# Kernel tuning notes

Measured on AMD Instinct MI355X. Metric: run time of the kernel, lower is better.

The kernel has to match this reference:

```python
import jax, jax.numpy as jnp
import numpy as np

S, B, F, H, L = 256, 64, 512, 512, 4
INV_SQRT_H = float(1.0 / np.sqrt(H))


def _ln(x, g, b, eps=1e-5):
    # torch nn.LayerNorm: biased variance, eps=1e-5
    mu = jnp.mean(x, axis=-1, keepdims=True)
    var = jnp.var(x, axis=-1, keepdims=True)
    return (x - mu) * jax.lax.rsqrt(var + eps) * g + b


def setup_inputs() -> dict:
    key = jax.random.key(0)
    k1, k2 = jax.random.split(key)
    x = jax.random.normal(k1, (S, B, F), dtype=jnp.float32)  # time-major [S,B,F]
    W = jax.random.normal(k2, (L, 6, F, H), dtype=jnp.float32) * 0.02  # q,k,v,i,f,o
    b = jnp.zeros((L, 6, H), jnp.float32)
    ln_g = jnp.ones((L, 6, H), jnp.float32)
    ln_b = jnp.zeros((L, 6, H), jnp.float32)
    return {"x": x, "W": W, "b": b, "ln_g": ln_g, "ln_b": ln_b}


def reference(x, W, b, ln_g, ln_b):
    # Dropout is identity (eval mode / p effectively 0).
    def step(carry, x_t):
        h, c, n = carry  # each [L,B,H]
        layer_input = x_t  # [B,F]
        hs, cs, ns = [], [], []
        for l in range(L):
            # all 6 gate projections in one einsum: [6,B,H]
            z = jnp.einsum('bf,gfh->gbh', layer_input, W[l]) + b[l][:, None, :]
            z = z.at[1].multiply(INV_SQRT_H)  # k = Wk(x)/sqrt(H) before LN
            z = _ln(z, ln_g[l][:, None, :], ln_b[l][:, None, :])
            q, k, v = z[0], z[1], z[2]
            i = jax.nn.sigmoid(z[3])
            f = jax.nn.sigmoid(z[4])
            o = jax.nn.sigmoid(z[5])
            # (k[:,:,None] @ v[:,None,:]).sum(dim=1) == k.sum(-1,keepdims)*v
            kv_sum = jnp.sum(k, axis=-1, keepdims=True) * v
            c_l = f * c[l] + i * kv_sum
            n_l = f * n[l] + i * k
            n_hat = n_l / (jnp.linalg.norm(n_l, axis=-1, keepdims=True) + 1e-8)
            h_l = o * jnp.tanh(q * n_hat)
            if l > 0:  # residual_conn
                h_l = h_l + layer_input
            layer_input = h_l
            hs.append(h_l); cs.append(c_l); ns.append(n_l)
        h = jnp.stack(hs); c = jnp.stack(cs); n = jnp.stack(ns)
        return (h, c, n), h[-1]

    init = tuple(jnp.zeros((L, B, H), x.dtype) for _ in range(3))
    (h, c, n), out = jax.lax.scan(step, init, x)  # out: [S,B,H] time-major
    return out, h, c, n
```

## Files before the change

kernel.cpp:

```cpp
#include <hip/hip_runtime.h>


typedef unsigned short u16;
typedef unsigned int   u32;
typedef short s8v __attribute__((ext_vector_type(8)));
typedef float f4v __attribute__((ext_vector_type(4)));

#define S_    256
#define B_    64
#define F_    512
#define H_    512
#define L_    4
#define NG    3072
#define RALL  16384
#define CH    16
#define INV_SQRT_H 0.044194173824159216f

__device__ __forceinline__ float bu2f(u16 u) {
    union { u32 i; float f; } z; z.i = ((u32)u) << 16; return z.f;
}
__device__ __forceinline__ u16 f2bf(float f) {
    union { float f; u32 i; } z; z.f = f;
    u32 r = (z.i + 0x7FFFu + ((z.i >> 16) & 1u)) >> 16;
    return (u16)r;
}
__device__ __forceinline__ float sigm(float x)  { return 1.0f / (1.0f + __expf(-x)); }
__device__ __forceinline__ float tanhf_(float x){ return 2.0f / (1.0f + __expf(-2.0f * x)) - 1.0f; }
__device__ __forceinline__ float wred64(float v) {
    #pragma unroll
    for (int m = 1; m < 64; m <<= 1) v += __shfl_xor(v, m);
    return v;
}
__device__ __forceinline__ void gl_lds16(const u16* g, u16* l) {
    __builtin_amdgcn_global_load_lds((const __attribute__((address_space(1))) u32*)g,
                                     (__attribute__((address_space(3))) u32*)l, 16, 0, 0);
}
__device__ __forceinline__ void unp8(uint4 u, float* f) {
    f[0] = bu2f((u16)(u.x & 0xffff)); f[1] = bu2f((u16)(u.x >> 16));
    f[2] = bu2f((u16)(u.y & 0xffff)); f[3] = bu2f((u16)(u.y >> 16));
    f[4] = bu2f((u16)(u.z & 0xffff)); f[5] = bu2f((u16)(u.z >> 16));
    f[6] = bu2f((u16)(u.w & 0xffff)); f[7] = bu2f((u16)(u.w >> 16));
}
__device__ __forceinline__ uint4 pck8(const float* f) {
    uint4 u;
    u.x = (u32)f2bf(f[0]) | ((u32)f2bf(f[1]) << 16);
    u.y = (u32)f2bf(f[2]) | ((u32)f2bf(f[3]) << 16);
    u.z = (u32)f2bf(f[4]) | ((u32)f2bf(f[5]) << 16);
    u.w = (u32)f2bf(f[6]) | ((u32)f2bf(f[7]) << 16);
    return u;
}

__global__ void convw_k(const float* __restrict__ W, u16* __restrict__ WT) {
    __shared__ float tile[32][33];
    const int lg = blockIdx.z;
    const int h0 = blockIdx.x * 32, f0 = blockIdx.y * 32;
    const float* Wb = W  + (size_t)lg * F_ * H_;
    u16*        WTb = WT + (size_t)lg * F_ * H_;
    const int tx = threadIdx.x, ty = threadIdx.y;
    #pragma unroll
    for (int i = 0; i < 32; i += 8)
        tile[ty + i][tx] = Wb[(size_t)(f0 + ty + i) * H_ + h0 + tx];
    __syncthreads();
    #pragma unroll
    for (int i = 0; i < 32; i += 8)
        WTb[(size_t)(h0 + ty + i) * F_ + f0 + tx] = f2bf(tile[tx][ty + i]);
}

__global__ void convx_k(const float* __restrict__ x, u16* __restrict__ A) {
    const int i = blockIdx.x * 256 + threadIdx.x;
    float4 v = ((const float4*)x)[i];
    u32 lo = (u32)f2bf(v.x) | ((u32)f2bf(v.y) << 16);
    u32 hi = (u32)f2bf(v.z) | ((u32)f2bf(v.w) << 16);
    ((uint2*)A)[i] = make_uint2(lo, hi);
}

__global__ __launch_bounds__(256) void gemm_k(const u16* __restrict__ A,
                                              const u16* __restrict__ BT,
                                              u16* __restrict__ Z,
                                              const float* __restrict__ bias,
                                              int arow0) {
    __shared__ u16 lsA[128 * 64];
    __shared__ u16 lsB[128 * 64];
    const int t = threadIdx.x;
    const int ntile = blockIdx.x;
    const int mtile = blockIdx.y;
    const int ncol0 = ntile * 128;
    const u16* Ab = A  + (size_t)(arow0 + mtile * 128) * F_;
    const u16* Bb = BT + (size_t)ntile * 128 * F_;
    const int lane = t & 63, wv = t >> 6;

    f4v acc[4][4];
    #pragma unroll
    for (int i = 0; i < 4; i++)
        #pragma unroll
        for (int j = 0; j < 4; j++) acc[i][j] = 0.0f;

    const int wm = (wv >> 1) * 64, wn = (wv & 1) * 64;
    const int ro = lane & 15, kq = lane >> 4;
    const int slot0 = kq ^ (ro & 7);
    const int slot1 = (kq + 4) ^ (ro & 7);

    int goff[4];
    #pragma unroll
    for (int s = 0; s < 4; s++) {
        const int c = t + 256 * s;
        const int row = c >> 3, slot = c & 7;
        const int g = slot ^ (row & 7);
        goff[s] = row * F_ + g * 8;
    }

    for (int kb = 0; kb < 8; ++kb) {
        const int kofs = kb * 64;
        #pragma unroll
        for (int s = 0; s < 4; s++) {
            const int c = t + 256 * s;
            gl_lds16(Ab + goff[s] + kofs, lsA + c * 8);
            gl_lds16(Bb + goff[s] + kofs, lsB + c * 8);
        }
        __syncthreads();
        #pragma unroll
        for (int kk = 0; kk < 2; ++kk) {
            const int slot = kk ? slot1 : slot0;
            s8v fa[4], fb[4];
            #pragma unroll
            for (int i = 0; i < 4; i++)
                fa[i] = *(const s8v*)(lsA + (wm + i * 16 + ro) * 64 + slot * 8);
            #pragma unroll
            for (int j = 0; j < 4; j++)
                fb[j] = *(const s8v*)(lsB + (wn + j * 16 + ro) * 64 + slot * 8);
            #pragma unroll
            for (int i = 0; i < 4; i++)
                #pragma unroll
                for (int j = 0; j < 4; j++)
                    acc[i][j] = __builtin_amdgcn_mfma_f32_16x16x32_bf16(fa[i], fb[j], acc[i][j], 0, 0, 0);
        }
        __syncthreads();
    }

    const int cl = lane & 15, rq = kq * 4;
    #pragma unroll
    for (int j = 0; j < 4; j++) {
        const int col = ncol0 + wn + j * 16 + cl;
        const float bv = bias[col];
        #pragma unroll
        for (int i = 0; i < 4; i++) {
            const int mbase = mtile * 128 + wm + i * 16 + rq;
            #pragma unroll
            for (int r2 = 0; r2 < 4; r2++)
                Z[(size_t)(mbase + r2) * NG + col] = f2bf(acc[i][j][r2] + bv);
        }
    }
}

__global__ __launch_bounds__(256) void stats_k(const u16* __restrict__ Z,
                                               const float* __restrict__ lng1,
                                               const float* __restrict__ lnb1,
                                               float* __restrict__ stats) {
    const int wid = threadIdx.x >> 6, lane = threadIdx.x & 63;
    const int row = blockIdx.x * 4 + wid;
    const u16* zr = Z + (size_t)row * NG + lane * 8;

    float g1v[8], b1v[8];
    #pragma unroll
    for (int j = 0; j < 8; j++) { g1v[j] = lng1[lane * 8 + j]; b1v[j] = lnb1[lane * 8 + j]; }

    float s[6], sq[6], wk = 0.f, sg1 = 0.f, sb1 = 0.f;
    #pragma unroll
    for (int g = 0; g < 6; ++g) {
        uint4 u = *(const uint4*)(zr + g * 512);
        float f[8];
        unp8(u, f);
        float ls = 0.f, lq = 0.f;
        #pragma unroll
        for (int j = 0; j < 8; j++) { ls += f[j]; lq += f[j] * f[j]; }
        s[g] = ls; sq[g] = lq;
        if (g == 1) {
            #pragma unroll
            for (int j = 0; j < 8; j++) wk += g1v[j] * f[j];
        }
    }
    #pragma unroll
    for (int j = 0; j < 8; j++) { sg1 += g1v[j]; sb1 += b1v[j]; }

    #pragma unroll
    for (int g = 0; g < 6; ++g) { s[g] = wred64(s[g]); sq[g] = wred64(sq[g]); }
    wk = wred64(wk); sg1 = wred64(sg1); sb1 = wred64(sb1);

    if (lane == 0) {
        float* o = stats + (size_t)row * 16;
        const float inv = 1.0f / 512.0f;
        float mu[6], rs[6];
        #pragma unroll
        for (int g = 0; g < 6; ++g) {
            float m = s[g] * inv, e2 = sq[g] * inv;
            if (g == 1) { m *= INV_SQRT_H; e2 *= INV_SQRT_H * INV_SQRT_H; }
            float var = fmaxf(e2 - m * m, 0.0f);
            mu[g] = m; rs[g] = rsqrtf(var + 1e-5f);
        }
        #pragma unroll
        for (int g = 0; g < 6; ++g) { o[g] = mu[g]; o[6 + g] = rs[g]; }
        o[12] = rs[1] * (INV_SQRT_H * wk - mu[1] * sg1) + sb1;
    }
}

__global__ __launch_bounds__(128) void scanA_k(const u16* __restrict__ Z,
                                               const float* __restrict__ stats,
                                               const float* __restrict__ lngl,
                                               const float* __restrict__ lnbl,
                                               u16* __restrict__ nbuf,
                                               u16* __restrict__ pbuf,
                                               float* __restrict__ sumP,
                                               float* __restrict__ sumC,
                                               float* __restrict__ sumN) {
    const int b = blockIdx.y, chunk = blockIdx.z;
    const int h = blockIdx.x * 128 + threadIdx.x;
    __shared__ float sst[CH][16];
    for (int i = threadIdx.x; i < CH * 16; i += 128) {
        const int tc = i >> 4, j = i & 15;
        sst[tc][j] = stats[(size_t)((chunk * CH + tc) * 64 + b) * 16 + j];
    }
    float gg[4], gb[4];
    #pragma unroll
    for (int g = 0; g < 4; ++g) {
        gg[g] = lngl[(g + 1) * 512 + h];
        gb[g] = lnbl[(g + 1) * 512 + h];
    }
    __syncthreads();

    float c = 0.f, n = 0.f, P = 1.f;
    #pragma unroll 4
    for (int tc = 0; tc < CH; ++tc) {
        const int r = (chunk * CH + tc) * 64 + b;
        const u16* zr = Z + (size_t)r * NG + h;
        const float z1 = bu2f(zr[512]);
        const float z2 = bu2f(zr[1024]);
        const float z3 = bu2f(zr[1536]);
        const float z4 = bu2f(zr[2048]);
        const float kk = (z1 * INV_SQRT_H - sst[tc][1]) * sst[tc][7] * gg[0] + gb[0];
        const float vv = (z2 - sst[tc][2]) * sst[tc][8]  * gg[1] + gb[1];
        const float ii = sigm((z3 - sst[tc][3]) * sst[tc][9]  * gg[2] + gb[2]);
        const float ff = sigm((z4 - sst[tc][4]) * sst[tc][10] * gg[3] + gb[3]);
        c = ff * c + ii * (sst[tc][12] * vv);
        n = ff * n + ii * kk;
        P *= ff;
        nbuf[(size_t)r * 512 + h] = f2bf(n);
        pbuf[(size_t)r * 512 + h] = f2bf(P);
    }
    const size_t idx = ((size_t)chunk << 15) + (b << 9) + h;
    sumP[idx] = P; sumC[idx] = c; sumN[idx] = n;
}

__global__ __launch_bounds__(256) void scanB_k(const float* __restrict__ sumP,
                                               const float* __restrict__ sumC,
                                               const float* __restrict__ sumN,
                                               float* __restrict__ n0buf,
                                               float* __restrict__ cstate,
                                               float* __restrict__ nstate,
                                               float* __restrict__ finals,
                                               int t0, int NC, int l) {
    const int idx = blockIdx.x * 256 + threadIdx.x;
    float c, n;
    if (t0 == 0) { c = 0.f; n = 0.f; }
    else { c = cstate[idx]; n = nstate[idx]; }
    for (int ch = 0; ch < NC; ++ch) {
        const size_t o = ((size_t)ch << 15) + idx;
        n0buf[o] = n;
        const float P = sumP[o];
        c = sumC[o] + P * c;
        n = sumN[o] + P * n;
    }
    if (t0 + NC * CH == S_) {
        const int b = idx >> 9, h = idx & 511;
        const size_t so = ((size_t)l * B_ + b) * H_ + h;
        finals[(size_t)L_ * B_ * H_ + so] = c;
        finals[(size_t)2 * L_ * B_ * H_ + so] = n;
    } else {
        cstate[idx] = c; nstate[idx] = n;
    }
}

__global__ __launch_bounds__(256) void normh_k(const u16* __restrict__ Z,
                                               const u16* __restrict__ nbuf,
                                               const u16* __restrict__ pbuf,
                                               const float* __restrict__ n0buf,
                                               const float* __restrict__ stats,
                                               const float* __restrict__ lngl,
                                               const float* __restrict__ lnbl,
                                               float* __restrict__ hbuf,
                                               u16* __restrict__ aoutB,
                                               float* __restrict__ outp,
                                               float* __restrict__ finals,
                                               int t0, int l) {
    const int wid = threadIdx.x >> 6, lane = threadIdx.x & 63;
    const int r = blockIdx.x * 4 + wid;
    const int h0 = lane * 8;

    float nl[8], pv[8];
    unp8(*(const uint4*)(nbuf + (size_t)r * 512 + h0), nl);
    unp8(*(const uint4*)(pbuf + (size_t)r * 512 + h0), pv);
    const float* n0r = n0buf + ((size_t)(r >> 10) << 15) + ((size_t)(r & 63) << 9) + h0;
    const float4 na = *(const float4*)(n0r);
    const float4 nb = *(const float4*)(n0r + 4);
    const float n0v[8] = {na.x, na.y, na.z, na.w, nb.x, nb.y, nb.z, nb.w};

    float nv[8], nsq = 0.f;
    #pragma unroll
    for (int j = 0; j < 8; j++) {
        nv[j] = fmaf(pv[j], n0v[j], nl[j]);
        nsq += nv[j] * nv[j];
    }
    nsq = wred64(nsq);
    const float rinv = 1.0f / (sqrtf(nsq) + 1e-8f);

    const u16* zr = Z + (size_t)r * NG;
    float z0[8], z5[8];
    unp8(*(const uint4*)(zr + h0), z0);
    unp8(*(const uint4*)(zr + 2560 + h0), z5);

    const float* st = stats + (size_t)r * 16;
    const float mu0 = st[0], rs0 = st[6], mu5 = st[5], rs5 = st[11];

    float g0[8], b0[8], g5[8], b5[8];
    #pragma unroll
    for (int j = 0; j < 8; j++) {
        g0[j] = lngl[h0 + j];        b0[j] = lnbl[h0 + j];
        g5[j] = lngl[2560 + h0 + j]; b5[j] = lnbl[2560 + h0 + j];
    }

    const int tl = r >> 6, b = r & 63;
    const int gr = t0 + tl;
    const size_t grow = (((size_t)gr * 64 + b) * 512) + h0;

    float hv[8];
    #pragma unroll
    for (int j = 0; j < 8; j++) {
        const float q  = (z0[j] - mu0) * rs0 * g0[j] + b0[j];
        const float oo = sigm((z5[j] - mu5) * rs5 * g5[j] + b5[j]);
        hv[j] = oo * tanhf_(q * nv[j] * rinv);
    }
    if (l > 0) {
        #pragma unroll
        for (int j = 0; j < 8; j++) hv[j] += hbuf[grow + j];
    }
    if (outp) {
        #pragma unroll
        for (int j = 0; j < 8; j++) outp[grow + j] = hv[j];
    } else {
        #pragma unroll
        for (int j = 0; j < 8; j++) hbuf[grow + j] = hv[j];
    }
    if (aoutB) *(uint4*)(aoutB + grow) = pck8(hv);

    if (gr == S_ - 1) {
        const size_t so = (((size_t)l * B_ + b) * 512) + h0;
        #pragma unroll
        for (int j = 0; j < 8; j++) finals[so + j] = hv[j];
    }
}

extern "C" void kernel_launch(void* const* d_in, const int* in_sizes, int n_in,
                              void* d_out, int out_size, void* d_ws, size_t ws_size,
                              hipStream_t stream) {
    const float* x   = (const float*)d_in[0];
    const float* W   = (const float*)d_in[1];
    const float* bia = (const float*)d_in[2];
    const float* lng = (const float*)d_in[3];
    const float* lnb = (const float*)d_in[4];
    float* out = (float*)d_out;

    const size_t WT_B = (size_t)L_ * 6 * H_ * F_ * 2;
    const size_t A_B  = (size_t)RALL * F_ * 2;
    const size_t ST_B = (size_t)RALL * 16 * 4;
    const size_t CS_B = (size_t)B_ * H_ * 4;
    const size_t HB_B = (size_t)RALL * H_ * 4;
    auto zB  = [](int T) { return (size_t)T * B_ * NG * 2; };
    auto nB  = [](int T) { return (size_t)T * B_ * H_ * 2; };
    auto cxB = [](int T) { return (size_t)(T / CH) * B_ * H_ * 4; };
    const size_t base = WT_B + A_B + ST_B + 2 * CS_B + HB_B + 32768;

    int T = 16;
    const int cand[3] = {256, 64, 16};
    for (int i = 0; i < 3; i++) {
        const int Tc = cand[i];
        if (ws_size >= base + zB(Tc) + 2 * nB(Tc) + 4 * cxB(Tc)) { T = Tc; break; }
    }
    const int NC = T / CH;

    char* ws = (char*)d_ws;
    size_t off = 0;
    auto take = [&](size_t nb) { size_t o = off; off += (nb + 255) & ~(size_t)255; return o; };
    u16*   WT    = (u16*)  (ws + take(WT_B));
    u16*   Abf   = (u16*)  (ws + take(A_B));
    float* stats = (float*)(ws + take(ST_B));
    float* cs    = (float*)(ws + take(CS_B));
    float* ns    = (float*)(ws + take(CS_B));
    float* hbuf  = (float*)(ws + take(HB_B));
    u16*   zb    = (u16*)  (ws + take(zB(T)));
    u16*   nbuf  = (u16*)  (ws + take(nB(T)));
    u16*   pbuf  = (u16*)  (ws + take(nB(T)));
    float* sumP  = (float*)(ws + take(cxB(T)));
    float* sumC  = (float*)(ws + take(cxB(T)));
    float* sumN  = (float*)(ws + take(cxB(T)));
    float* n0buf = (float*)(ws + take(cxB(T)));

    convw_k<<<dim3(16, 16, 24), dim3(32, 8), 0, stream>>>(W, WT);
    convx_k<<<dim3(RALL * F_ / 4 / 256), dim3(256), 0, stream>>>(x, Abf);

    float* finals = out + (size_t)S_ * B_ * H_;
    for (int l = 0; l < L_; ++l) {
        const u16*   WTl   = WT  + (size_t)l * 6 * H_ * F_;
        const float* biasl = bia + (size_t)l * NG;
        const float* lngl  = lng + (size_t)l * 6 * H_;
        const float* lnbl  = lnb + (size_t)l * 6 * H_;
        for (int j = 0; j < S_ / T; ++j) {
            const int t0 = j * T, arow0 = t0 * B_;
            const int rows = T * B_;
            gemm_k<<<dim3(24, rows / 128), dim3(256), 0, stream>>>(Abf, WTl, zb, biasl, arow0);
            stats_k<<<dim3(rows / 4), dim3(256), 0, stream>>>(zb, lngl + H_, lnbl + H_, stats);
            scanA_k<<<dim3(4, B_, NC), dim3(128), 0, stream>>>(zb, stats, lngl, lnbl,
                                                               nbuf, pbuf, sumP, sumC, sumN);
            scanB_k<<<dim3(128), dim3(256), 0, stream>>>(sumP, sumC, sumN, n0buf,
                                                         cs, ns, finals, t0, NC, l);
            normh_k<<<dim3(rows / 4), dim3(256), 0, stream>>>(zb, nbuf, pbuf, n0buf, stats,
                                                              lngl, lnbl, hbuf,
                                                              (l < 3) ? Abf : (u16*)nullptr,
                                                              (l == 3) ? out : (float*)nullptr,
                                                              finals, t0, l);
        }
    }
}
```

Before: 680.1 us.

## Switch GEMM to 32x32x16 MFMA and move q/o LayerNorm stats into normh

The GEMM now uses 32x32x16 bf16 MFMA with 2x2 accumulator tiles per wave instead of 4x4 tiles of 16x16x32, which halves the LDS fragment loads per k-step. The epilogue is remapped to the 32x32 output layout. stats_k now computes statistics only for gates k,v,i,f, and normh_k computes the q and o gate mean/rstd itself from values it already loads, dropping its stats read. The 32x32 epilogue writes rows with a different stride pattern, which may change store coalescing.

```diff
diff --git a/kernel.cpp b/kernel.cpp
--- a/kernel.cpp
+++ b/kernel.cpp
@@ -3,8 +3,8 @@
 
 typedef unsigned short u16;
 typedef unsigned int   u32;
-typedef short s8v __attribute__((ext_vector_type(8)));
-typedef float f4v __attribute__((ext_vector_type(4)));
+typedef short s8v  __attribute__((ext_vector_type(8)));
+typedef float f16v __attribute__((ext_vector_type(16)));
 
 #define S_    256
 #define B_    64
@@ -89,16 +89,15 @@
     const u16* Bb = BT + (size_t)ntile * 128 * F_;
     const int lane = t & 63, wv = t >> 6;
 
-    f4v acc[4][4];
-    #pragma unroll
-    for (int i = 0; i < 4; i++)
-        #pragma unroll
-        for (int j = 0; j < 4; j++) acc[i][j] = 0.0f;
+    f16v acc[2][2];
+    #pragma unroll
+    for (int i = 0; i < 2; i++)
+        #pragma unroll
+        for (int j = 0; j < 2; j++) acc[i][j] = 0.0f;
 
     const int wm = (wv >> 1) * 64, wn = (wv & 1) * 64;
-    const int ro = lane & 15, kq = lane >> 4;
-    const int slot0 = kq ^ (ro & 7);
-    const int slot1 = (kq + 4) ^ (ro & 7);
+    const int rl = lane & 31, hi = lane >> 5;
+    const int r7 = rl & 7;
 
     int goff[4];
     #pragma unroll
@@ -119,35 +118,36 @@
         }
         __syncthreads();
         #pragma unroll
-        for (int kk = 0; kk < 2; ++kk) {
-            const int slot = kk ? slot1 : slot0;
-            s8v fa[4], fb[4];
+        for (int s = 0; s < 4; ++s) {
+            const int slot = ((s << 1) + hi) ^ r7;
+            s8v fa[2], fb[2];
             #pragma unroll
-            for (int i = 0; i < 4; i++)
-                fa[i] = *(const s8v*)(lsA + (wm + i * 16 + ro) * 64 + slot * 8);
+            for (int i = 0; i < 2; i++)
+                fa[i] = *(const s8v*)(lsA + (wm + i * 32 + rl) * 64 + slot * 8);
             #pragma unroll
-            for (int j = 0; j < 4; j++)
-                fb[j] = *(const s8v*)(lsB + (wn + j * 16 + ro) * 64 + slot * 8);
+            for (int j = 0; j < 2; j++)
+                fb[j] = *(const s8v*)(lsB + (wn + j * 32 + rl) * 64 + slot * 8);
             #pragma unroll
-            for (int i = 0; i < 4; i++)
+            for (int i = 0; i < 2; i++)
                 #pragma unroll
-                for (int j = 0; j < 4; j++)
-                    acc[i][j] = __builtin_amdgcn_mfma_f32_16x16x32_bf16(fa[i], fb[j], acc[i][j], 0, 0, 0);
+                for (int j = 0; j < 2; j++)
+                    acc[i][j] = __builtin_amdgcn_mfma_f32_32x32x16_bf16(fa[i], fb[j], acc[i][j], 0, 0, 0);
         }
         __syncthreads();
     }
 
-    const int cl = lane & 15, rq = kq * 4;
-    #pragma unroll
-    for (int j = 0; j < 4; j++) {
-        const int col = ncol0 + wn + j * 16 + cl;
+    #pragma unroll
+    for (int j = 0; j < 2; j++) {
+        const int col = ncol0 + wn + j * 32 + rl;
         const float bv = bias[col];
         #pragma unroll
-        for (int i = 0; i < 4; i++) {
-            const int mbase = mtile * 128 + wm + i * 16 + rq;
+        for (int i = 0; i < 2; i++) {
+            const int mbase = mtile * 128 + wm + i * 32 + hi * 4;
             #pragma unroll
-            for (int r2 = 0; r2 < 4; r2++)
-                Z[(size_t)(mbase + r2) * NG + col] = f2bf(acc[i][j][r2] + bv);
+            for (int reg = 0; reg < 16; reg++) {
+                const int row = mbase + (reg & 3) + 8 * (reg >> 2);
+                Z[(size_t)row * NG + col] = f2bf(acc[i][j][reg] + bv);
+            }
         }
     }
 }
@@ -164,17 +164,17 @@
     #pragma unroll
     for (int j = 0; j < 8; j++) { g1v[j] = lng1[lane * 8 + j]; b1v[j] = lnb1[lane * 8 + j]; }
 
-    float s[6], sq[6], wk = 0.f, sg1 = 0.f, sb1 = 0.f;
-    #pragma unroll
-    for (int g = 0; g < 6; ++g) {
-        uint4 u = *(const uint4*)(zr + g * 512);
+    float s[4], sq[4], wk = 0.f, sg1 = 0.f, sb1 = 0.f;
+    #pragma unroll
+    for (int g = 0; g < 4; ++g) {
+        uint4 u = *(const uint4*)(zr + (g + 1) * 512);
         float f[8];
         unp8(u, f);
         float ls = 0.f, lq = 0.f;
         #pragma unroll
         for (int j = 0; j < 8; j++) { ls += f[j]; lq += f[j] * f[j]; }
         s[g] = ls; sq[g] = lq;
-        if (g == 1) {
+        if (g == 0) {
             #pragma unroll
             for (int j = 0; j < 8; j++) wk += g1v[j] * f[j];
         }
@@ -183,23 +183,22 @@
     for (int j = 0; j < 8; j++) { sg1 += g1v[j]; sb1 += b1v[j]; }
 
     #pragma unroll
-    for (int g = 0; g < 6; ++g) { s[g] = wred64(s[g]); sq[g] = wred64(sq[g]); }
+    for (int g = 0; g < 4; ++g) { s[g] = wred64(s[g]); sq[g] = wred64(sq[g]); }
     wk = wred64(wk); sg1 = wred64(sg1); sb1 = wred64(sb1);
 
     if (lane == 0) {
         float* o = stats + (size_t)row * 16;
         const float inv = 1.0f / 512.0f;
-        float mu[6], rs[6];
-        #pragma unroll
-        for (int g = 0; g < 6; ++g) {
+        float mu1 = 0.f, rs1 = 0.f;
+        #pragma unroll
+        for (int g = 0; g < 4; ++g) {
             float m = s[g] * inv, e2 = sq[g] * inv;
-            if (g == 1) { m *= INV_SQRT_H; e2 *= INV_SQRT_H * INV_SQRT_H; }
-            float var = fmaxf(e2 - m * m, 0.0f);
-            mu[g] = m; rs[g] = rsqrtf(var + 1e-5f);
-        }
-        #pragma unroll
-        for (int g = 0; g < 6; ++g) { o[g] = mu[g]; o[6 + g] = rs[g]; }
-        o[12] = rs[1] * (INV_SQRT_H * wk - mu[1] * sg1) + sb1;
+            if (g == 0) { m *= INV_SQRT_H; e2 *= INV_SQRT_H * INV_SQRT_H; }
+            const float rs = rsqrtf(fmaxf(e2 - m * m, 0.0f) + 1e-5f);
+            o[1 + g] = m; o[7 + g] = rs;
+            if (g == 0) { mu1 = m; rs1 = rs; }
+        }
+        o[12] = rs1 * (INV_SQRT_H * wk - mu1 * sg1) + sb1;
     }
 }
 
@@ -283,7 +282,6 @@
                                                const u16* __restrict__ nbuf,
                                                const u16* __restrict__ pbuf,
                                                const float* __restrict__ n0buf,
-                                               const float* __restrict__ stats,
                                                const float* __restrict__ lngl,
                                                const float* __restrict__ lnbl,
                                                float* __restrict__ hbuf,
@@ -303,22 +301,28 @@
     const float4 nb = *(const float4*)(n0r + 4);
     const float n0v[8] = {na.x, na.y, na.z, na.w, nb.x, nb.y, nb.z, nb.w};
 
-    float nv[8], nsq = 0.f;
-    #pragma unroll
-    for (int j = 0; j < 8; j++) {
-        nv[j] = fmaf(pv[j], n0v[j], nl[j]);
-        nsq += nv[j] * nv[j];
-    }
-    nsq = wred64(nsq);
-    const float rinv = 1.0f / (sqrtf(nsq) + 1e-8f);
-
     const u16* zr = Z + (size_t)r * NG;
     float z0[8], z5[8];
     unp8(*(const uint4*)(zr + h0), z0);
     unp8(*(const uint4*)(zr + 2560 + h0), z5);
 
-    const float* st = stats + (size_t)r * 16;
-    const float mu0 = st[0], rs0 = st[6], mu5 = st[5], rs5 = st[11];
+    float nsq = 0.f, s0 = 0.f, q0 = 0.f, s5 = 0.f, q5 = 0.f;
+    float nv[8];
+    #pragma unroll
+    for (int j = 0; j < 8; j++) {
+        nv[j] = fmaf(pv[j], n0v[j], nl[j]);
+        nsq += nv[j] * nv[j];
+        s0 += z0[j]; q0 += z0[j] * z0[j];
+        s5 += z5[j]; q5 += z5[j] * z5[j];
+    }
+    nsq = wred64(nsq);
+    s0 = wred64(s0); q0 = wred64(q0);
+    s5 = wred64(s5); q5 = wred64(q5);
+    const float rinv = 1.0f / (sqrtf(nsq) + 1e-8f);
+    const float inv = 1.0f / 512.0f;
+    const float mu0 = s0 * inv, mu5 = s5 * inv;
+    const float rs0 = rsqrtf(fmaxf(q0 * inv - mu0 * mu0, 0.0f) + 1e-5f);
+    const float rs5 = rsqrtf(fmaxf(q5 * inv - mu5 * mu5, 0.0f) + 1e-5f);
 
     float g0[8], b0[8], g5[8], b5[8];
     #pragma unroll
@@ -421,7 +425,7 @@
                                                                nbuf, pbuf, sumP, sumC, sumN);
             scanB_k<<<dim3(128), dim3(256), 0, stream>>>(sumP, sumC, sumN, n0buf,
                                                          cs, ns, finals, t0, NC, l);
-            normh_k<<<dim3(rows / 4), dim3(256), 0, stream>>>(zb, nbuf, pbuf, n0buf, stats,
+            normh_k<<<dim3(rows / 4), dim3(256), 0, stream>>>(zb, nbuf, pbuf, n0buf,
                                                               lngl, lnbl, hbuf,
                                                               (l < 3) ? Abf : (u16*)nullptr,
                                                               (l == 3) ? out : (float*)nullptr,
```

After: 632.6 us. 1.08x faster.
